# Performance work log

Measured on AMD Instinct MI355X. Metric: run time of the kernel, lower is better.

The kernel has to match this reference:

```python
import jax, jax.numpy as jnp
import numpy as np

NUM_HEADS = 16


def setup_inputs() -> dict:
    key = jax.random.key(0)
    k1, k2, k3, k4 = jax.random.split(key, 4)
    in_dim, out_dim = 1024, 1024
    x = jax.random.normal(k1, (4, 2048, in_dim), dtype=jnp.float32)
    # nn.Linear weights stored as [out, in]; we keep that convention.
    s = 1.0 / np.sqrt(in_dim)
    Wq = jax.random.uniform(k2, (out_dim, in_dim), jnp.float32, -s, s)
    Wk = jax.random.uniform(k3, (out_dim, in_dim), jnp.float32, -s, s)
    Wv = jax.random.uniform(k4, (out_dim, in_dim), jnp.float32, -s, s)
    return {"x": x, "Wq": Wq, "Wk": Wk, "Wv": Wv}


def reference(x, Wq, Wk, Wv):
    b, n, _ = x.shape
    out_dim = Wq.shape[0]
    h = NUM_HEADS
    d = out_dim // h  # head_dim

    def split_heads(t):  # [b,n,out] -> [b,h,n,d]
        return t.reshape(b, n, h, d).transpose(0, 2, 1, 3)

    q = split_heads(x @ Wq.T)
    k = split_heads(x @ Wk.T)
    v = split_heads(x @ Wv.T)

    scores = jnp.einsum("bhqd,bhkd->bhqk", q, k) / jnp.sqrt(jnp.float32(d))
    causal = jnp.tril(jnp.ones((n, n), dtype=bool))
    scores = jnp.where(causal, scores, -jnp.inf)
    attn = jax.nn.softmax(scores, axis=-1)
    out = jnp.einsum("bhqk,bhkd->bhqd", attn, v)
    return out.transpose(0, 2, 1, 3).reshape(b, n, out_dim)
```

## Files before the change

### kernel.cpp

```cpp
#include <hip/hip_runtime.h>

typedef __attribute__((ext_vector_type(8))) short short8;
typedef __attribute__((ext_vector_type(4))) short short4v;
typedef __attribute__((ext_vector_type(4))) float floatx4;

#define GLOBAL_AS __attribute__((address_space(1)))
#define LDS_AS __attribute__((address_space(3)))

__device__ __forceinline__ short f2bs(float f) {
    union { float f; unsigned u; } v; v.f = f;
    unsigned r = v.u + 0x7fffu + ((v.u >> 16) & 1u);
    return (short)(r >> 16);
}

__device__ __forceinline__ short f2bs_fast(float f) {
    union { float f; unsigned u; } v; v.f = f;
    return (short)((v.u + 0x8000u) >> 16);
}

__global__ __launch_bounds__(256) void cast_all(const float* __restrict__ x,
                                                const float* __restrict__ Wq,
                                                const float* __restrict__ Wk,
                                                const float* __restrict__ Wv,
                                                short* __restrict__ xb,
                                                short* __restrict__ wb) {
    int b = blockIdx.x;
    int t = threadIdx.x;
    const float* src;
    short* dst;
    int idx;
    if (b < 8192) {
        src = x; dst = xb; idx = b * 1024 + t * 4;
    } else {
        int r = b - 8192;
        int wz = r >> 10;
        src = (wz == 0) ? Wq : (wz == 1) ? Wk : Wv;
        dst = wb + wz * (1 << 20);
        idx = (r & 1023) * 1024 + t * 4;
    }
    float4 v = *(const float4*)(src + idx);
    short4v o;
    o.x = f2bs(v.x); o.y = f2bs(v.y); o.z = f2bs(v.z); o.w = f2bs(v.w);
    *(short4v*)(dst + idx) = o;
}

__global__ __launch_bounds__(256) void qkv_gemm(const short* __restrict__ xb,
                                                const short* __restrict__ wb,
                                                short* __restrict__ qout,
                                                short* __restrict__ kout,
                                                short* __restrict__ vtout) {
    __shared__ short As[128 * 64];
    __shared__ short Bs[128 * 64];
    const int K = 1024;
    int tid = threadIdx.x;
    int lane = tid & 63;
    int wid = tid >> 6;
    int quad = lane >> 4;
    int l16 = lane & 15;
    int wm = (wid >> 1) * 64;
    int wn = (wid & 1) * 64;
    int bm = blockIdx.x * 128;
    int bn = blockIdx.y * 128;
    const short* W = wb + (size_t)blockIdx.z * K * 1024;

    floatx4 acc[4][4];
#pragma unroll
    for (int i = 0; i < 4; i++)
#pragma unroll
        for (int j = 0; j < 4; j++) acc[i][j] = (floatx4){0.f, 0.f, 0.f, 0.f};

    int srow = tid >> 3;
    int ssw = ((tid & 7) ^ (srow & 7)) * 8;

    for (int kk = 0; kk < K; kk += 64) {
        __syncthreads();
#pragma unroll
        for (int l = 0; l < 4; l++) {
            const short* g = xb + (size_t)(bm + srow + l * 32) * K + kk + ssw;
            __builtin_amdgcn_global_load_lds((const GLOBAL_AS void*)g,
                                             (LDS_AS void*)(As + tid * 8 + l * 2048), 16, 0, 0);
        }
#pragma unroll
        for (int l = 0; l < 4; l++) {
            const short* g = W + (size_t)(bn + srow + l * 32) * K + kk + ssw;
            __builtin_amdgcn_global_load_lds((const GLOBAL_AS void*)g,
                                             (LDS_AS void*)(Bs + tid * 8 + l * 2048), 16, 0, 0);
        }
        __syncthreads();

#pragma unroll
        for (int s = 0; s < 2; s++) {
            int slot = ((s * 4 + quad) ^ (l16 & 7)) * 8;
            short8 af[4], bf[4];
#pragma unroll
            for (int i = 0; i < 4; i++)
                af[i] = *(const short8*)(As + (wm + i * 16 + l16) * 64 + slot);
#pragma unroll
            for (int j = 0; j < 4; j++)
                bf[j] = *(const short8*)(Bs + (wn + j * 16 + l16) * 64 + slot);
#pragma unroll
            for (int i = 0; i < 4; i++)
#pragma unroll
                for (int j = 0; j < 4; j++)
                    acc[i][j] = __builtin_amdgcn_mfma_f32_16x16x32_bf16(af[i], bf[j], acc[i][j], 0, 0, 0);
        }
    }

    if (blockIdx.z == 2) {
#pragma unroll
        for (int i = 0; i < 4; i++) {
#pragma unroll
            for (int j = 0; j < 4; j++) {
                int m = bm + wm + i * 16 + quad * 4;
                int c = bn + wn + j * 16 + l16;
                int b = m >> 11, nn = m & 2047, h = c >> 6, dd = c & 63;
                short4v pk;
                pk.x = f2bs(acc[i][j][0]);
                pk.y = f2bs(acc[i][j][1]);
                pk.z = f2bs(acc[i][j][2]);
                pk.w = f2bs(acc[i][j][3]);
                *(short4v*)(vtout + ((size_t)(b * 16 + h) * 64 + dd) * 2048 + nn) = pk;
            }
        }
    } else {
        short* dst = (blockIdx.z == 0) ? qout : kout;
        float qs = (blockIdx.z == 0) ? 0.180336881f : 1.0f;
#pragma unroll
        for (int i = 0; i < 4; i++) {
#pragma unroll
            for (int j = 0; j < 4; j++) {
#pragma unroll
                for (int r = 0; r < 4; r++) {
                    int m = bm + wm + i * 16 + quad * 4 + r;
                    int c = bn + wn + j * 16 + l16;
                    dst[((size_t)((m >> 11) * 16 + (c >> 6)) * 2048 + (m & 2047)) * 64 + (c & 63)] =
                        f2bs(acc[i][j][r] * qs);
                }
            }
        }
    }
}

__global__ __launch_bounds__(256) void attn(const short* __restrict__ q,
                                            const short* __restrict__ k,
                                            const short* __restrict__ vt,
                                            float* __restrict__ out) {
    __shared__ short Ks[128 * 64];
    __shared__ short Vs[64 * 128];
    __shared__ short Ps[4 * 16 * 136];

    int tid = threadIdx.x;
    int lane = tid & 63;
    int wid = tid >> 6;
    int quad = lane >> 4;
    int l16 = lane & 15;

    int flat = blockIdx.x;
    int xcd = flat & 7;
    int slot = flat >> 3;
    int bh = xcd * 8 + (slot >> 4);
    int qx = slot & 15;
    int b = bh >> 4, h = bh & 15;

    const short* qp = q + (size_t)(b * 16 + h) * 2048 * 64;
    const short* kp = k + (size_t)(b * 16 + h) * 2048 * 64;
    const short* vp = vt + (size_t)(b * 16 + h) * 64 * 2048;

    int krow = tid >> 3;
    int ksw = ((tid & 7) ^ (krow & 7)) * 8;
    int vd = tid >> 4;
    int vc = tid & 15;
    int vsw = ((vc & 8) | ((vc ^ vd) & 7)) * 8;

    short* pw = Ps + wid * (16 * 136);

    short8 ones;
#pragma unroll
    for (int i = 0; i < 8; i++) ones[i] = (short)0x3F80;

    for (int phase = 0; phase < 2; phase++) {
        int qt = (phase == 0) ? qx : (31 - qx);
        int qbase = qt * 64;
        int qrow_w = qbase + wid * 16;

        short8 qf0 = *(const short8*)(qp + (size_t)(qrow_w + l16) * 64 + quad * 8);
        short8 qf1 = *(const short8*)(qp + (size_t)(qrow_w + l16) * 64 + 32 + quad * 8);

        floatx4 oacc[4];
#pragma unroll
        for (int d = 0; d < 4; d++) oacc[d] = (floatx4){0.f, 0.f, 0.f, 0.f};
        floatx4 lacc = (floatx4){0.f, 0.f, 0.f, 0.f};

        int ntiles = (qt >> 1) + 1;
        for (int t = 0; t < ntiles; t++) {
            int kvb = t * 128;
            __syncthreads();
#pragma unroll
            for (int l = 0; l < 4; l++) {
                const short* g = kp + (size_t)(kvb + krow + l * 32) * 64 + ksw;
                __builtin_amdgcn_global_load_lds((const GLOBAL_AS void*)g,
                                                 (LDS_AS void*)(Ks + tid * 8 + l * 2048), 16, 0, 0);
            }
#pragma unroll
            for (int l = 0; l < 4; l++) {
                const short* g = vp + (size_t)(vd + l * 16) * 2048 + kvb + vsw;
                __builtin_amdgcn_global_load_lds((const GLOBAL_AS void*)g,
                                                 (LDS_AS void*)(Vs + tid * 8 + l * 2048), 16, 0, 0);
            }
            __syncthreads();

            floatx4 sacc[8];
#pragma unroll
            for (int j = 0; j < 8; j++) sacc[j] = (floatx4){0.f, 0.f, 0.f, 0.f};
#pragma unroll
            for (int s = 0; s < 2; s++) {
#pragma unroll
                for (int j = 0; j < 8; j++) {
                    int row = j * 16 + l16;
                    short8 kf = *(const short8*)(Ks + row * 64 +
                                                 (((s * 4 + quad) ^ (row & 7)) * 8));
                    sacc[j] = __builtin_amdgcn_mfma_f32_16x16x32_bf16(
                        (s == 0) ? qf0 : qf1, kf, sacc[j], 0, 0, 0);
                }
            }

            bool diag = (kvb + 127 > qrow_w);
#pragma unroll
            for (int r = 0; r < 4; r++) {
                int qr = qrow_w + quad * 4 + r;
#pragma unroll
                for (int j = 0; j < 8; j++) {
                    float p = __builtin_amdgcn_exp2f(sacc[j][r]);
                    if (diag) p = (kvb + j * 16 + l16 > qr) ? 0.f : p;
                    pw[(quad * 4 + r) * 136 + j * 16 + l16] = f2bs_fast(p);
                }
            }
            __threadfence_block();

#pragma unroll
            for (int s = 0; s < 4; s++) {
                short8 pf = *(const short8*)(pw + l16 * 136 + s * 32 + quad * 8);
                lacc = __builtin_amdgcn_mfma_f32_16x16x32_bf16(pf, ones, lacc, 0, 0, 0);
#pragma unroll
                for (int d = 0; d < 4; d++) {
                    int row = d * 16 + l16;
                    int c = s * 4 + quad;
                    int slotv = (c & 8) | ((c ^ (row & 7)) & 7);
                    short8 vf = *(const short8*)(Vs + row * 128 + slotv * 8);
                    oacc[d] = __builtin_amdgcn_mfma_f32_16x16x32_bf16(pf, vf, oacc[d], 0, 0, 0);
                }
            }
        }

        float inv[4];
#pragma unroll
        for (int r = 0; r < 4; r++) inv[r] = 1.0f / lacc[r];

#pragma unroll
        for (int d = 0; d < 4; d++) {
#pragma unroll
            for (int r = 0; r < 4; r++) {
                int nn = qrow_w + quad * 4 + r;
                out[((size_t)b * 2048 + nn) * 1024 + h * 64 + d * 16 + l16] = oacc[d][r] * inv[r];
            }
        }
    }
}

extern "C" void kernel_launch(void* const* d_in, const int* in_sizes, int n_in,
                              void* d_out, int out_size, void* d_ws, size_t ws_size,
                              hipStream_t stream) {
    const float* x = (const float*)d_in[0];
    const float* Wq = (const float*)d_in[1];
    const float* Wk = (const float*)d_in[2];
    const float* Wv = (const float*)d_in[3];
    float* out = (float*)d_out;
    char* ws = (char*)d_ws;

    short* xb = (short*)ws;
    short* wb = (short*)(ws + (16u << 20));
    short* qb = (short*)(ws + (22u << 20));
    short* kb = (short*)(ws + (38u << 20));
    short* vtb = (short*)(ws + (54u << 20));

    cast_all<<<8192 + 3 * 1024, 256, 0, stream>>>(x, Wq, Wk, Wv, xb, wb);
    qkv_gemm<<<dim3(64, 8, 3), 256, 0, stream>>>(xb, wb, qb, kb, vtb);
    attn<<<1024, 256, 0, stream>>>(qb, kb, vtb, out);
}
```

Before: 242.5 us.

## Rewrite attention with 32x32x16 MFMA and 128-row query tiles per block

Restructures the attention kernel so each wave handles 32 query rows using 32x32x16 bf16 MFMAs, computing S transposed (K as A operand) and doubling the query tile per block to 128 rows, which halves the grid to 512 blocks and reuses each K/V tile across twice as many queries. The row-sum is now accumulated in registers instead of through an extra MFMA against a ones vector, P is packed with a hardware bf16 pack conversion when available, and the causal mask is applied only on the last tile. The cost is more registers per thread (16-wide accumulators) and fewer blocks, which risks lower occupancy and worse load balance.

```diff
diff --git a/kernel.cpp b/kernel.cpp
--- a/kernel.cpp
+++ b/kernel.cpp
@@ -3,6 +3,7 @@
 typedef __attribute__((ext_vector_type(8))) short short8;
 typedef __attribute__((ext_vector_type(4))) short short4v;
 typedef __attribute__((ext_vector_type(4))) float floatx4;
+typedef __attribute__((ext_vector_type(16))) float floatx16;
 
 #define GLOBAL_AS __attribute__((address_space(1)))
 #define LDS_AS __attribute__((address_space(3)))
@@ -13,10 +14,19 @@
     return (short)(r >> 16);
 }
 
-__device__ __forceinline__ short f2bs_fast(float f) {
-    union { float f; unsigned u; } v; v.f = f;
-    return (short)((v.u + 0x8000u) >> 16);
-}
+#if __has_builtin(__builtin_amdgcn_cvt_pk_bf16_f32)
+typedef __attribute__((ext_vector_type(2))) __bf16 bf16x2;
+__device__ __forceinline__ unsigned pk2(float a, float b) {
+    union { bf16x2 v; unsigned u; } u;
+    u.v = __builtin_amdgcn_cvt_pk_bf16_f32(a, b);
+    return u.u;
+}
+#else
+__device__ __forceinline__ unsigned pk2(float a, float b) {
+    union { float f; unsigned u; } x, y; x.f = a; y.f = b;
+    return ((y.u + 0x8000u) & 0xffff0000u) | ((x.u + 0x8000u) >> 16);
+}
+#endif
 
 __global__ __launch_bounds__(256) void cast_all(const float* __restrict__ x,
                                                 const float* __restrict__ Wq,
@@ -141,25 +151,25 @@
     }
 }
 
-__global__ __launch_bounds__(256) void attn(const short* __restrict__ q,
-                                            const short* __restrict__ k,
-                                            const short* __restrict__ vt,
-                                            float* __restrict__ out) {
+__global__ __launch_bounds__(256, 2) void attn(const short* __restrict__ q,
+                                               const short* __restrict__ k,
+                                               const short* __restrict__ vt,
+                                               float* __restrict__ out) {
     __shared__ short Ks[128 * 64];
     __shared__ short Vs[64 * 128];
-    __shared__ short Ps[4 * 16 * 136];
+    __shared__ short Ps[4 * 32 * 136];
 
     int tid = threadIdx.x;
     int lane = tid & 63;
     int wid = tid >> 6;
-    int quad = lane >> 4;
-    int l16 = lane & 15;
+    int l32 = lane & 31;
+    int half = lane >> 5;
 
     int flat = blockIdx.x;
     int xcd = flat & 7;
     int slot = flat >> 3;
-    int bh = xcd * 8 + (slot >> 4);
-    int qx = slot & 15;
+    int bh = xcd * 8 + (slot >> 3);
+    int qx = slot & 7;
     int b = bh >> 4, h = bh & 15;
 
     const short* qp = q + (size_t)(b * 16 + h) * 2048 * 64;
@@ -172,26 +182,27 @@
     int vc = tid & 15;
     int vsw = ((vc & 8) | ((vc ^ vd) & 7)) * 8;
 
-    short* pw = Ps + wid * (16 * 136);
-
-    short8 ones;
-#pragma unroll
-    for (int i = 0; i < 8; i++) ones[i] = (short)0x3F80;
+    short* pw = Ps + wid * (32 * 136);
 
     for (int phase = 0; phase < 2; phase++) {
-        int qt = (phase == 0) ? qx : (31 - qx);
-        int qbase = qt * 64;
-        int qrow_w = qbase + wid * 16;
-
-        short8 qf0 = *(const short8*)(qp + (size_t)(qrow_w + l16) * 64 + quad * 8);
-        short8 qf1 = *(const short8*)(qp + (size_t)(qrow_w + l16) * 64 + 32 + quad * 8);
-
-        floatx4 oacc[4];
-#pragma unroll
-        for (int d = 0; d < 4; d++) oacc[d] = (floatx4){0.f, 0.f, 0.f, 0.f};
-        floatx4 lacc = (floatx4){0.f, 0.f, 0.f, 0.f};
-
-        int ntiles = (qt >> 1) + 1;
+        int qt = (phase == 0) ? qx : (15 - qx);
+        int qbase = qt * 128;
+        int qrow_w = qbase + wid * 32;
+        int qlane = qrow_w + l32;
+
+        short8 qf[4];
+#pragma unroll
+        for (int s = 0; s < 4; s++)
+            qf[s] = *(const short8*)(qp + (size_t)qlane * 64 + s * 16 + half * 8);
+
+        floatx16 oacc[2];
+#pragma unroll
+        for (int nt = 0; nt < 2; nt++)
+#pragma unroll
+            for (int e = 0; e < 16; e++) oacc[nt][e] = 0.f;
+        float rs = 0.f;
+
+        int ntiles = qt + 1;
         for (int t = 0; t < ntiles; t++) {
             int kvb = t * 128;
             __syncthreads();
@@ -209,59 +220,72 @@
             }
             __syncthreads();
 
-            floatx4 sacc[8];
-#pragma unroll
-            for (int j = 0; j < 8; j++) sacc[j] = (floatx4){0.f, 0.f, 0.f, 0.f};
-#pragma unroll
-            for (int s = 0; s < 2; s++) {
-#pragma unroll
-                for (int j = 0; j < 8; j++) {
-                    int row = j * 16 + l16;
-                    short8 kf = *(const short8*)(Ks + row * 64 +
-                                                 (((s * 4 + quad) ^ (row & 7)) * 8));
-                    sacc[j] = __builtin_amdgcn_mfma_f32_16x16x32_bf16(
-                        (s == 0) ? qf0 : qf1, kf, sacc[j], 0, 0, 0);
-                }
-            }
-
-            bool diag = (kvb + 127 > qrow_w);
-#pragma unroll
-            for (int r = 0; r < 4; r++) {
-                int qr = qrow_w + quad * 4 + r;
-#pragma unroll
-                for (int j = 0; j < 8; j++) {
-                    float p = __builtin_amdgcn_exp2f(sacc[j][r]);
-                    if (diag) p = (kvb + j * 16 + l16 > qr) ? 0.f : p;
-                    pw[(quad * 4 + r) * 136 + j * 16 + l16] = f2bs_fast(p);
+            floatx16 sacc[4];
+#pragma unroll
+            for (int kb = 0; kb < 4; kb++)
+#pragma unroll
+                for (int e = 0; e < 16; e++) sacc[kb][e] = 0.f;
+#pragma unroll
+            for (int s = 0; s < 4; s++) {
+#pragma unroll
+                for (int kb = 0; kb < 4; kb++) {
+                    int key = kb * 32 + l32;
+                    int c = s * 2 + half;
+                    short8 kf = *(const short8*)(Ks + key * 64 + ((c ^ (key & 7)) * 8));
+                    sacc[kb] = __builtin_amdgcn_mfma_f32_32x32x16_bf16(kf, qf[s], sacc[kb], 0, 0, 0);
+                }
+            }
+
+            bool diag = (t == ntiles - 1) && (phase >= 0) && (kvb + 127 > qrow_w);
+#pragma unroll
+            for (int kb = 0; kb < 4; kb++) {
+#pragma unroll
+                for (int e = 0; e < 16; e++) {
+                    float p = __builtin_amdgcn_exp2f(sacc[kb][e]);
+                    if (diag) {
+                        int key = kvb + kb * 32 + (e & 3) + 8 * (e >> 2) + 4 * half;
+                        p = (key > qlane) ? 0.f : p;
+                    }
+                    sacc[kb][e] = p;
+                    rs += p;
+                }
+#pragma unroll
+                for (int g = 0; g < 4; g++) {
+                    int2 wv;
+                    wv.x = pk2(sacc[kb][4 * g], sacc[kb][4 * g + 1]);
+                    wv.y = pk2(sacc[kb][4 * g + 2], sacc[kb][4 * g + 3]);
+                    *(int2*)(pw + l32 * 136 + kb * 32 + g * 8 + 4 * half) = wv;
                 }
             }
             __threadfence_block();
 
 #pragma unroll
-            for (int s = 0; s < 4; s++) {
-                short8 pf = *(const short8*)(pw + l16 * 136 + s * 32 + quad * 8);
-                lacc = __builtin_amdgcn_mfma_f32_16x16x32_bf16(pf, ones, lacc, 0, 0, 0);
-#pragma unroll
-                for (int d = 0; d < 4; d++) {
-                    int row = d * 16 + l16;
-                    int c = s * 4 + quad;
-                    int slotv = (c & 8) | ((c ^ (row & 7)) & 7);
-                    short8 vf = *(const short8*)(Vs + row * 128 + slotv * 8);
-                    oacc[d] = __builtin_amdgcn_mfma_f32_16x16x32_bf16(pf, vf, oacc[d], 0, 0, 0);
-                }
-            }
-        }
-
-        float inv[4];
-#pragma unroll
-        for (int r = 0; r < 4; r++) inv[r] = 1.0f / lacc[r];
-
-#pragma unroll
-        for (int d = 0; d < 4; d++) {
-#pragma unroll
-            for (int r = 0; r < 4; r++) {
-                int nn = qrow_w + quad * 4 + r;
-                out[((size_t)b * 2048 + nn) * 1024 + h * 64 + d * 16 + l16] = oacc[d][r] * inv[r];
+            for (int s = 0; s < 8; s++) {
+                short8 pf = *(const short8*)(pw + l32 * 136 + s * 16 + half * 8);
+#pragma unroll
+                for (int nt = 0; nt < 2; nt++) {
+                    int d = nt * 32 + l32;
+                    int c = s * 2 + half;
+                    int sl = (c & 8) | ((c ^ (d & 7)) & 7);
+                    short8 vf = *(const short8*)(Vs + d * 128 + sl * 8);
+                    oacc[nt] = __builtin_amdgcn_mfma_f32_32x32x16_bf16(pf, vf, oacc[nt], 0, 0, 0);
+                }
+            }
+        }
+
+        float tot = rs + __shfl_xor(rs, 32);
+        float inv = 1.0f / tot;
+        float invr[16];
+#pragma unroll
+        for (int e = 0; e < 16; e++)
+            invr[e] = __shfl(inv, (e & 3) + 8 * (e >> 2) + 4 * half);
+#pragma unroll
+        for (int nt = 0; nt < 2; nt++) {
+#pragma unroll
+            for (int e = 0; e < 16; e++) {
+                int r = (e & 3) + 8 * (e >> 2) + 4 * half;
+                int nn = qrow_w + r;
+                out[((size_t)b * 2048 + nn) * 1024 + h * 64 + nt * 32 + l32] = oacc[nt][e] * invr[e];
             }
         }
     }
@@ -285,5 +309,5 @@
 
     cast_all<<<8192 + 3 * 1024, 256, 0, stream>>>(x, Wq, Wk, Wv, xb, wb);
     qkv_gemm<<<dim3(64, 8, 3), 256, 0, stream>>>(xb, wb, qb, kb, vtb);
-    attn<<<1024, 256, 0, stream>>>(qb, kb, vtb, out);
-}
+    attn<<<512, 256, 0, stream>>>(qb, kb, vtb, out);
+}
```

Result: faster. 205.3 us (-15.4%).
